# Optimization experiments

Measured on AMD Instinct MI355X. Metric: run time of the kernel, lower is better.

The kernel has to match this reference:

```python
import jax, jax.numpy as jnp
import numpy as np

B, T, H, E = 256, 512, 512, 32

def setup_inputs() -> dict:
    key = jax.random.key(0)
    ks = jax.random.split(key, 7)
    events = jax.random.randint(ks[0], (B, T), 0, E, dtype=jnp.int32)
    # strictly increasing event times (as produced by cumsum of positive gaps upstream)
    gaps = jax.random.uniform(ks[1], (B, T), dtype=jnp.float32) * 0.1 + 1e-3
    times = jnp.cumsum(gaps, axis=1)
    emb = jax.random.normal(ks[2], (E, H), dtype=jnp.float32) * 0.05
    # 5 gate Linears (input, forget, output, cell, decay) stacked: [2H, 5H]
    W_gates = jax.random.normal(ks[3], (2 * H, 5 * H), dtype=jnp.float32) * (1.0 / np.sqrt(2 * H))
    b_gates = jnp.zeros((5 * H,), dtype=jnp.float32)
    W_int = jax.random.normal(ks[4], (H, E), dtype=jnp.float32) * (1.0 / np.sqrt(H))
    b_int = jnp.zeros((E,), dtype=jnp.float32)
    return {"events": events, "times": times, "emb": emb,
            "W_gates": W_gates, "b_gates": b_gates, "W_int": W_int, "b_int": b_int}

def reference(events, times, emb, W_gates, b_gates, W_int, b_int):
    Bs, Ts = events.shape
    Hs = emb.shape[1]
    x_seq = emb[events]                                   # [B,T,H] embedding lookup
    deltas = jnp.concatenate([times[:, :1], jnp.diff(times, axis=1)], axis=1)  # [B,T]
    xs = (jnp.transpose(x_seq, (1, 0, 2)), deltas.T)      # ([T,B,H], [T,B])

    def step(carry, inp):
        h, c = carry
        x, dt = inp
        comb = jnp.concatenate([x, h], axis=1)            # [B,2H]
        g = comb @ W_gates + b_gates                      # [B,5H] fused gate GEMM
        i, f, o, c_tilde, d = jnp.split(g, 5, axis=1)
        i, f, o, c_tilde = jnp.tanh(i), jnp.tanh(f), jnp.tanh(o), jnp.tanh(c_tilde)
        decay = jax.nn.softplus(d)
        c_dec = c * jnp.exp(-decay * dt[:, None])
        c_n = f * c_dec + i * c_tilde
        h_n = o * jnp.tanh(c_n)
        lam = jax.nn.softplus(h_n @ W_int + b_int)        # [B,E]
        return (h_n, c_n), (lam, h_n)

    h0 = jnp.zeros((Bs, Hs), dtype=times.dtype)
    c0 = jnp.zeros((Bs, Hs), dtype=times.dtype)
    _, (lams, hs) = jax.lax.scan(step, (h0, c0), xs)
    intensities = jnp.transpose(lams, (1, 0, 2))          # [B,T,E]
    hidden_states = jnp.transpose(hs, (1, 0, 2))          # [B,T,H]
    return intensities, hidden_states
```

## Files before the change

### kernel.cpp

```cpp
#include <hip/hip_runtime.h>
#include <math.h>


#define Bb   256
#define Tt   512
#define Hh   512
#define Ee   32
#define G5H  2560
#define NTHR 256
#define RT   16
#define CT   32

typedef __attribute__((ext_vector_type(8))) short f16x8;
typedef __attribute__((ext_vector_type(4))) float f32x4;

__device__ __forceinline__ float softplusf(float x) {
    return fmaxf(x, 0.f) + __logf(1.f + __expf(-fabsf(x)));
}
__device__ __forceinline__ float fast_tanh(float x) {
    const float t = fminf(fmaxf(x, -15.f), 15.f);
    const float e = __expf(2.f * t);
    return (e - 1.f) / (e + 1.f);
}
__device__ __forceinline__ unsigned short f2h(float f) {
    _Float16 h = (_Float16)f;
    return *reinterpret_cast<unsigned short*>(&h);
}

__device__ __forceinline__ void load_a4(const unsigned short* p, f16x8 (&a)[4]) {
    asm volatile(
        "global_load_dwordx4 %0, %4, off sc0 sc1\n\t"
        "global_load_dwordx4 %1, %4, off offset:64 sc0 sc1\n\t"
        "global_load_dwordx4 %2, %4, off offset:128 sc0 sc1\n\t"
        "global_load_dwordx4 %3, %4, off offset:192 sc0 sc1\n\t"
        "s_waitcnt vmcnt(0)"
        : "=&v"(a[0]), "=&v"(a[1]), "=&v"(a[2]), "=&v"(a[3])
        : "v"(p) : "memory");
}
__device__ __forceinline__ void st_u32_sc(void* p, unsigned v) {
    asm volatile("global_store_dword %0, %1, off sc0 sc1"
                 :: "v"(p), "v"(v) : "memory");
}

__global__ __launch_bounds__(NTHR, 1)
void nhp_scan(const int* __restrict__ events, const float* __restrict__ times,
              const float* __restrict__ emb, const float* __restrict__ Wg,
              const float* __restrict__ bg, float* __restrict__ out_hid,
              unsigned* __restrict__ cnt, unsigned short* __restrict__ hb) {
    __shared__ float red[4][10][16][18];
    __shared__ float gx[Ee][5][34];
    __shared__ int   ev_s[RT];
    __shared__ float dt_s[RT];

    const int tid  = threadIdx.x, bid = blockIdx.x;
    const int rt   = bid & 15;
    const int ct   = bid >> 4;
    const int r0   = rt * RT;
    const int lane = tid & 63;
    const int ks   = tid >> 6;
    const int frow = lane & 15, kgrp = lane >> 4;
    const int erow = tid >> 4;
    const int ecp  = (tid & 15) * 2;

    for (int u = tid; u < Ee * 5 * CT; u += NTHR) {
        const int e = u / 160, r = u - e * 160;
        const int g = r >> 5, hc = r & 31;
        const int gcol = g * Hh + ct * CT + hc;
        float acc = bg[gcol];
        const float* er = emb + (size_t)e * Hh;
        for (int k = 0; k < Hh; k += 4) {
            acc += er[k]     * Wg[(size_t)k       * G5H + gcol];
            acc += er[k + 1] * Wg[(size_t)(k + 1) * G5H + gcol];
            acc += er[k + 2] * Wg[(size_t)(k + 2) * G5H + gcol];
            acc += er[k + 3] * Wg[(size_t)(k + 3) * G5H + gcol];
        }
        gx[e][g][hc] = acc;
    }

    f16x8 Bf[10][4];
    #pragma unroll
    for (int n = 0; n < 10; ++n) {
        const int col = (n >> 1) * Hh + ct * CT + (n & 1) * 16 + frow;
        #pragma unroll
        for (int kk = 0; kk < 4; ++kk) {
            const int k0 = ks * 128 + kk * 32 + kgrp * 8;
            union { f16x8 v; unsigned u[4]; } tmp;
            #pragma unroll
            for (int r = 0; r < 4; ++r) {
                const float w0 = Wg[(size_t)(Hh + k0 + 2 * r)     * G5H + col];
                const float w1 = Wg[(size_t)(Hh + k0 + 2 * r + 1) * G5H + col];
                tmp.u[r] = (unsigned)f2h(w0) | ((unsigned)f2h(w1) << 16);
            }
            Bf[n][kk] = tmp.v;
        }
    }

    float cA = 0.f, cB = 0.f;
    __syncthreads();

    for (int p = 0; p < Tt; ++p) {
        if (tid < RT) {
            const int b = r0 + tid;
            ev_s[tid] = events[b * Tt + p];
            const float tp = times[b * Tt + p];
            dt_s[tid] = (p == 0) ? tp : tp - times[b * Tt + p - 1];
        }

        if (p > 0) {
            const unsigned short* hprev = hb + (size_t)((p - 1) & 1) * Bb * Hh
                                        + (size_t)(r0 + frow) * Hh + ks * 128 + kgrp * 8;
            f16x8 a[4];
            load_a4(hprev, a);
            f32x4 acc[10];
            #pragma unroll
            for (int n = 0; n < 10; ++n) acc[n] = (f32x4){0.f, 0.f, 0.f, 0.f};
            #pragma unroll
            for (int kk = 0; kk < 4; ++kk) {
                #pragma unroll
                for (int n = 0; n < 10; ++n)
                    acc[n] = __builtin_amdgcn_mfma_f32_16x16x32_f16(
                        a[kk], Bf[n][kk], acc[n], 0, 0, 0);
            }
            #pragma unroll
            for (int n = 0; n < 10; ++n)
                #pragma unroll
                for (int r = 0; r < 4; ++r)
                    red[ks][n][kgrp * 4 + r][frow] = acc[n][r];
        }
        __syncthreads();

        const int   e  = ev_s[erow];
        const float dt = dt_s[erow];
        float hn[2];
        {
            float v0[5], v1[5];
            const int tl0 = ecp >> 4, fc = ecp & 15;
            #pragma unroll
            for (int gt = 0; gt < 5; ++gt) {
                const float2 gv = *(const float2*)&gx[e][gt][ecp];
                v0[gt] = gv.x; v1[gt] = gv.y;
                if (p > 0) {
                    const int tl = gt * 2 + tl0;
                    #pragma unroll
                    for (int s = 0; s < 4; ++s) {
                        const float2 pr = *(const float2*)&red[s][tl][erow][fc];
                        v0[gt] += pr.x; v1[gt] += pr.y;
                    }
                }
            }
            #pragma unroll
            for (int q = 0; q < 2; ++q) {
                const float* v = q ? v1 : v0;
                const float ig  = fast_tanh(v[0]);
                const float fg  = fast_tanh(v[1]);
                const float og  = fast_tanh(v[2]);
                const float ctl = fast_tanh(v[3]);
                const float dec = softplusf(v[4]);
                const float cpv = q ? cB : cA;
                const float cn  = fg * (cpv * __expf(-dec * dt)) + ig * ctl;
                if (q) cB = cn; else cA = cn;
                hn[q] = og * fast_tanh(cn);
            }
        }

        const unsigned pk = (unsigned)f2h(hn[0]) | ((unsigned)f2h(hn[1]) << 16);
        st_u32_sc(hb + (size_t)(p & 1) * Bb * Hh
                     + (size_t)(r0 + erow) * Hh + ct * CT + ecp, pk);
        asm volatile("s_waitcnt vmcnt(0)" ::: "memory");
        __syncthreads();

        if (tid == 0)
            (void)__hip_atomic_fetch_add(&cnt[rt * 16], 1u, __ATOMIC_RELAXED,
                                         __HIP_MEMORY_SCOPE_AGENT);

        float2 ho; ho.x = hn[0]; ho.y = hn[1];
        *(float2*)(out_hid + ((size_t)(r0 + erow) * Tt + p) * Hh + ct * CT + ecp) = ho;

        if (tid == 0) {
            const unsigned target = 16u * (unsigned)(p + 1);
            int guard = 0;
            while (__hip_atomic_load(&cnt[rt * 16], __ATOMIC_RELAXED,
                                     __HIP_MEMORY_SCOPE_AGENT) < target) {
                if (++guard > 2000000) break;
            }
        }
        __syncthreads();
    }
}

__global__ __launch_bounds__(NTHR)
void nhp_intens(const float* __restrict__ out_hid, const float* __restrict__ Wi,
                const float* __restrict__ bi, float* __restrict__ out_int) {
    __shared__ float lred[32][8][32];
    const int tid = threadIdx.x;
    const int seg = tid >> 5, e = tid & 31;
    const size_t row0 = (size_t)blockIdx.x * 32;

    float w[64];
    #pragma unroll
    for (int j = 0; j < 64; ++j) w[j] = Wi[(size_t)(seg * 64 + j) * Ee + e];

    for (int r = 0; r < 32; ++r) {
        const float* hp = out_hid + (row0 + r) * Hh + seg * 64;
        float a0 = 0.f, a1 = 0.f;
        #pragma unroll
        for (int k = 0; k < 64; k += 4) {
            const float4 hv = *(const float4*)(hp + k);
            a0 += hv.x * w[k]     + hv.y * w[k + 1];
            a1 += hv.z * w[k + 2] + hv.w * w[k + 3];
        }
        lred[r][seg][e] = a0 + a1;
    }
    __syncthreads();
    #pragma unroll
    for (int c = 0; c < 4; ++c) {
        const int r = c * 8 + (tid >> 5);
        float s = bi[e];
        #pragma unroll
        for (int i = 0; i < 8; ++i) s += lred[r][i][e];
        out_int[(row0 + r) * Ee + e] = softplusf(s);
    }
}

extern "C" void kernel_launch(void* const* d_in, const int* in_sizes, int n_in,
                              void* d_out, int out_size, void* d_ws, size_t ws_size,
                              hipStream_t stream) {
    const int*   events = (const int*)d_in[0];
    const float* times  = (const float*)d_in[1];
    const float* emb    = (const float*)d_in[2];
    const float* Wg     = (const float*)d_in[3];
    const float* bg     = (const float*)d_in[4];
    const float* Wi     = (const float*)d_in[5];
    const float* bi     = (const float*)d_in[6];
    float* out_int = (float*)d_out;
    float* out_hid = out_int + (size_t)Bb * Tt * Ee;
    unsigned* cnt = (unsigned*)d_ws;
    unsigned short* hb = (unsigned short*)((char*)d_ws + 4096);

    hipMemsetAsync(d_ws, 0, 4096, stream);
    hipLaunchKernelGGL(nhp_scan, dim3(256), dim3(NTHR), 0, stream,
                       events, times, emb, Wg, bg, out_hid, cnt, hb);
    hipLaunchKernelGGL(nhp_intens, dim3((Bb * Tt) / 32), dim3(NTHR), 0, stream,
                       out_hid, Wi, bi, out_int);
}
```

Baseline: 2.527 ms.

## Replace per-step atomic barrier with tagged hidden-state polling; MFMA intensity kernel

Drops the per-timestep atomic counter barrier and its two block-wide syncs. Each hidden-state dword is now stored together with a step tag, and consumers poll their own A-fragment loads until every tag matches the current step. The reduction and event buffers are double-buffered, the gx LDS layout is XOR-swizzled to avoid bank conflicts, and the intensity projection is rewritten to use f16 MFMA. The trade-off is twice the global traffic for the h exchange, spin-polling that could livelock or fall back on timeout, and fp16 rounding in the intensity GEMM.

```diff
diff --git a/kernel.cpp b/kernel.cpp
--- a/kernel.cpp
+++ b/kernel.cpp
@@ -13,6 +13,8 @@
 
 typedef __attribute__((ext_vector_type(8))) short f16x8;
 typedef __attribute__((ext_vector_type(4))) float f32x4;
+typedef __attribute__((ext_vector_type(4))) unsigned u32x4;
+typedef __attribute__((ext_vector_type(2))) unsigned u32x2;
 
 __device__ __forceinline__ float softplusf(float x) {
     return fmaxf(x, 0.f) + __logf(1.f + __expf(-fabsf(x)));
@@ -27,18 +29,24 @@
     return *reinterpret_cast<unsigned short*>(&h);
 }
 
-__device__ __forceinline__ void load_a4(const unsigned short* p, f16x8 (&a)[4]) {
+__device__ __forceinline__ void load_tagged8(const unsigned* p, u32x4 (&d)[8]) {
     asm volatile(
-        "global_load_dwordx4 %0, %4, off sc0 sc1\n\t"
-        "global_load_dwordx4 %1, %4, off offset:64 sc0 sc1\n\t"
-        "global_load_dwordx4 %2, %4, off offset:128 sc0 sc1\n\t"
-        "global_load_dwordx4 %3, %4, off offset:192 sc0 sc1\n\t"
+        "global_load_dwordx4 %0, %8, off sc0 sc1\n\t"
+        "global_load_dwordx4 %1, %8, off offset:16 sc0 sc1\n\t"
+        "global_load_dwordx4 %2, %8, off offset:128 sc0 sc1\n\t"
+        "global_load_dwordx4 %3, %8, off offset:144 sc0 sc1\n\t"
+        "global_load_dwordx4 %4, %8, off offset:256 sc0 sc1\n\t"
+        "global_load_dwordx4 %5, %8, off offset:272 sc0 sc1\n\t"
+        "global_load_dwordx4 %6, %8, off offset:384 sc0 sc1\n\t"
+        "global_load_dwordx4 %7, %8, off offset:400 sc0 sc1\n\t"
         "s_waitcnt vmcnt(0)"
-        : "=&v"(a[0]), "=&v"(a[1]), "=&v"(a[2]), "=&v"(a[3])
+        : "=&v"(d[0]), "=&v"(d[1]), "=&v"(d[2]), "=&v"(d[3]),
+          "=&v"(d[4]), "=&v"(d[5]), "=&v"(d[6]), "=&v"(d[7])
         : "v"(p) : "memory");
 }
-__device__ __forceinline__ void st_u32_sc(void* p, unsigned v) {
-    asm volatile("global_store_dword %0, %1, off sc0 sc1"
+__device__ __forceinline__ void store_tagged(unsigned* p, unsigned data, unsigned tag) {
+    u32x2 v; v.x = data; v.y = tag;
+    asm volatile("global_store_dwordx2 %0, %1, off sc0 sc1"
                  :: "v"(p), "v"(v) : "memory");
 }
 
@@ -46,11 +54,11 @@
 void nhp_scan(const int* __restrict__ events, const float* __restrict__ times,
               const float* __restrict__ emb, const float* __restrict__ Wg,
               const float* __restrict__ bg, float* __restrict__ out_hid,
-              unsigned* __restrict__ cnt, unsigned short* __restrict__ hb) {
-    __shared__ float red[4][10][16][18];
+              unsigned* __restrict__ hb) {
+    __shared__ float red[2][4][10][16][18];
     __shared__ float gx[Ee][5][34];
-    __shared__ int   ev_s[RT];
-    __shared__ float dt_s[RT];
+    __shared__ int   ev_s[2][RT];
+    __shared__ float dt_s[2][RT];
 
     const int tid  = threadIdx.x, bid = blockIdx.x;
     const int rt   = bid & 15;
@@ -74,7 +82,7 @@
             acc += er[k + 2] * Wg[(size_t)(k + 2) * G5H + gcol];
             acc += er[k + 3] * Wg[(size_t)(k + 3) * G5H + gcol];
         }
-        gx[e][g][hc] = acc;
+        gx[e][g][hc ^ ((e & 7) << 2)] = acc;
     }
 
     f16x8 Bf[10][4];
@@ -99,18 +107,38 @@
     __syncthreads();
 
     for (int p = 0; p < Tt; ++p) {
+        const int par = p & 1;
         if (tid < RT) {
             const int b = r0 + tid;
-            ev_s[tid] = events[b * Tt + p];
+            ev_s[par][tid] = events[b * Tt + p];
             const float tp = times[b * Tt + p];
-            dt_s[tid] = (p == 0) ? tp : tp - times[b * Tt + p - 1];
+            dt_s[par][tid] = (p == 0) ? tp : tp - times[b * Tt + p - 1];
         }
 
         if (p > 0) {
-            const unsigned short* hprev = hb + (size_t)((p - 1) & 1) * Bb * Hh
-                                        + (size_t)(r0 + frow) * Hh + ks * 128 + kgrp * 8;
+            const unsigned* base = hb + ((size_t)((p - 1) & 1) * Bb * 256
+                                 + (size_t)(r0 + frow) * 256 + ks * 64 + kgrp * 4) * 2;
+            const unsigned want = (unsigned)p;
+            u32x4 d[8];
+            int guard = 0;
+            for (;;) {
+                load_tagged8(base, d);
+                int ok = 1;
+                #pragma unroll
+                for (int i = 0; i < 8; ++i)
+                    ok &= (d[i].y == want) & (d[i].w == want);
+                if (__all(ok)) break;
+                if (++guard > 100000) break;
+                __builtin_amdgcn_s_sleep(1);
+            }
             f16x8 a[4];
-            load_a4(hprev, a);
+            #pragma unroll
+            for (int kk = 0; kk < 4; ++kk) {
+                union { f16x8 v; unsigned u[4]; } t;
+                t.u[0] = d[2 * kk].x;     t.u[1] = d[2 * kk].z;
+                t.u[2] = d[2 * kk + 1].x; t.u[3] = d[2 * kk + 1].z;
+                a[kk] = t.v;
+            }
             f32x4 acc[10];
             #pragma unroll
             for (int n = 0; n < 10; ++n) acc[n] = (f32x4){0.f, 0.f, 0.f, 0.f};
@@ -125,25 +153,26 @@
             for (int n = 0; n < 10; ++n)
                 #pragma unroll
                 for (int r = 0; r < 4; ++r)
-                    red[ks][n][kgrp * 4 + r][frow] = acc[n][r];
+                    red[par][ks][n][kgrp * 4 + r][frow] = acc[n][r];
         }
         __syncthreads();
 
-        const int   e  = ev_s[erow];
-        const float dt = dt_s[erow];
+        const int   e  = ev_s[par][erow];
+        const float dt = dt_s[par][erow];
+        const int   sc = (e & 7) << 2;
         float hn[2];
         {
             float v0[5], v1[5];
             const int tl0 = ecp >> 4, fc = ecp & 15;
             #pragma unroll
             for (int gt = 0; gt < 5; ++gt) {
-                const float2 gv = *(const float2*)&gx[e][gt][ecp];
+                const float2 gv = *(const float2*)&gx[e][gt][ecp ^ sc];
                 v0[gt] = gv.x; v1[gt] = gv.y;
                 if (p > 0) {
                     const int tl = gt * 2 + tl0;
                     #pragma unroll
                     for (int s = 0; s < 4; ++s) {
-                        const float2 pr = *(const float2*)&red[s][tl][erow][fc];
+                        const float2 pr = *(const float2*)&red[par][s][tl][erow][fc];
                         v0[gt] += pr.x; v1[gt] += pr.y;
                     }
                 }
@@ -164,61 +193,62 @@
         }
 
         const unsigned pk = (unsigned)f2h(hn[0]) | ((unsigned)f2h(hn[1]) << 16);
-        st_u32_sc(hb + (size_t)(p & 1) * Bb * Hh
-                     + (size_t)(r0 + erow) * Hh + ct * CT + ecp, pk);
-        asm volatile("s_waitcnt vmcnt(0)" ::: "memory");
-        __syncthreads();
-
-        if (tid == 0)
-            (void)__hip_atomic_fetch_add(&cnt[rt * 16], 1u, __ATOMIC_RELAXED,
-                                         __HIP_MEMORY_SCOPE_AGENT);
+        store_tagged(hb + ((size_t)par * Bb * 256 + (size_t)(r0 + erow) * 256
+                           + ct * 16 + (ecp >> 1)) * 2, pk, (unsigned)(p + 1));
 
         float2 ho; ho.x = hn[0]; ho.y = hn[1];
         *(float2*)(out_hid + ((size_t)(r0 + erow) * Tt + p) * Hh + ct * CT + ecp) = ho;
-
-        if (tid == 0) {
-            const unsigned target = 16u * (unsigned)(p + 1);
-            int guard = 0;
-            while (__hip_atomic_load(&cnt[rt * 16], __ATOMIC_RELAXED,
-                                     __HIP_MEMORY_SCOPE_AGENT) < target) {
-                if (++guard > 2000000) break;
-            }
-        }
-        __syncthreads();
     }
 }
 
 __global__ __launch_bounds__(NTHR)
 void nhp_intens(const float* __restrict__ out_hid, const float* __restrict__ Wi,
                 const float* __restrict__ bi, float* __restrict__ out_int) {
-    __shared__ float lred[32][8][32];
-    const int tid = threadIdx.x;
-    const int seg = tid >> 5, e = tid & 31;
-    const size_t row0 = (size_t)blockIdx.x * 32;
-
-    float w[64];
+    const int tid  = threadIdx.x;
+    const int w    = tid >> 6;
+    const int lane = tid & 63;
+    const int col  = lane & 15, kgrp = lane >> 4;
+
+    f16x8 Bfi[2][16];
     #pragma unroll
-    for (int j = 0; j < 64; ++j) w[j] = Wi[(size_t)(seg * 64 + j) * Ee + e];
-
-    for (int r = 0; r < 32; ++r) {
-        const float* hp = out_hid + (row0 + r) * Hh + seg * 64;
-        float a0 = 0.f, a1 = 0.f;
-        #pragma unroll
-        for (int k = 0; k < 64; k += 4) {
-            const float4 hv = *(const float4*)(hp + k);
-            a0 += hv.x * w[k]     + hv.y * w[k + 1];
-            a1 += hv.z * w[k + 2] + hv.w * w[k + 3];
-        }
-        lred[r][seg][e] = a0 + a1;
-    }
-    __syncthreads();
+    for (int n = 0; n < 2; ++n)
+        #pragma unroll
+        for (int kk = 0; kk < 16; ++kk) {
+            const int k0 = kk * 32 + kgrp * 8;
+            union { f16x8 v; unsigned u[4]; } tmp;
+            #pragma unroll
+            for (int r = 0; r < 4; ++r) {
+                const float w0 = Wi[(size_t)(k0 + 2 * r)     * Ee + n * 16 + col];
+                const float w1 = Wi[(size_t)(k0 + 2 * r + 1) * Ee + n * 16 + col];
+                tmp.u[r] = (unsigned)f2h(w0) | ((unsigned)f2h(w1) << 16);
+            }
+            Bfi[n][kk] = tmp.v;
+        }
+    const float bv[2] = { bi[col], bi[16 + col] };
+
     #pragma unroll
-    for (int c = 0; c < 4; ++c) {
-        const int r = c * 8 + (tid >> 5);
-        float s = bi[e];
-        #pragma unroll
-        for (int i = 0; i < 8; ++i) s += lred[r][i][e];
-        out_int[(row0 + r) * Ee + e] = softplusf(s);
+    for (int it = 0; it < 2; ++it) {
+        const size_t rowbase = (size_t)blockIdx.x * 128 + (w * 2 + it) * 16;
+        f32x4 acc0 = (f32x4){0.f,0.f,0.f,0.f}, acc1 = acc0;
+        #pragma unroll
+        for (int kk = 0; kk < 16; ++kk) {
+            const float* hp = out_hid + (rowbase + (lane & 15)) * Hh + kk * 32 + kgrp * 8;
+            const float4 hA = *(const float4*)hp;
+            const float4 hB = *(const float4*)(hp + 4);
+            union { f16x8 v; unsigned u[4]; } t;
+            t.u[0] = (unsigned)f2h(hA.x) | ((unsigned)f2h(hA.y) << 16);
+            t.u[1] = (unsigned)f2h(hA.z) | ((unsigned)f2h(hA.w) << 16);
+            t.u[2] = (unsigned)f2h(hB.x) | ((unsigned)f2h(hB.y) << 16);
+            t.u[3] = (unsigned)f2h(hB.z) | ((unsigned)f2h(hB.w) << 16);
+            acc0 = __builtin_amdgcn_mfma_f32_16x16x32_f16(t.v, Bfi[0][kk], acc0, 0, 0, 0);
+            acc1 = __builtin_amdgcn_mfma_f32_16x16x32_f16(t.v, Bfi[1][kk], acc1, 0, 0, 0);
+        }
+        #pragma unroll
+        for (int i = 0; i < 4; ++i) {
+            const size_t row = rowbase + kgrp * 4 + i;
+            out_int[row * Ee + col]      = softplusf(acc0[i] + bv[0]);
+            out_int[row * Ee + 16 + col] = softplusf(acc1[i] + bv[1]);
+        }
     }
 }
 
@@ -234,12 +264,11 @@
     const float* bi     = (const float*)d_in[6];
     float* out_int = (float*)d_out;
     float* out_hid = out_int + (size_t)Bb * Tt * Ee;
-    unsigned* cnt = (unsigned*)d_ws;
-    unsigned short* hb = (unsigned short*)((char*)d_ws + 4096);
-
-    hipMemsetAsync(d_ws, 0, 4096, stream);
+    unsigned* hb = (unsigned*)d_ws;
+
+    hipMemsetAsync(hb, 0, 2u * Bb * 256 * 8, stream);
     hipLaunchKernelGGL(nhp_scan, dim3(256), dim3(NTHR), 0, stream,
-                       events, times, emb, Wg, bg, out_hid, cnt, hb);
-    hipLaunchKernelGGL(nhp_intens, dim3((Bb * Tt) / 32), dim3(NTHR), 0, stream,
+                       events, times, emb, Wg, bg, out_hid, hb);
+    hipLaunchKernelGGL(nhp_intens, dim3((Bb * Tt) / 128), dim3(NTHR), 0, stream,
                        out_hid, Wi, bi, out_int);
 }
```

Measured after the change: 2.469 ms. -2.3%, faster.
